# Kernel optimization log

Hardware: AMD Instinct MI355X
Metric: run time of the kernel (lower is better)

## Reference

```python
import jax, jax.numpy as jnp
import numpy as np

KERNEL_SIZE = 5
SIGMA_SPACE = 1.0
SIGMA_COLOR = 0.1
PAD = KERNEL_SIZE // 2


def make_spatial_kernel(kernel_size, sigma_space):
    r = kernel_size // 2
    coords = jnp.arange(-r, r + 1, dtype=jnp.float32)
    xx, yy = jnp.meshgrid(coords, coords, indexing='ij')
    return jnp.exp(-(xx ** 2 + yy ** 2) / (2.0 * sigma_space ** 2))  # [K, K]


def setup_inputs() -> dict:
    key = jax.random.key(0)
    x = jax.random.uniform(key, (4, 3, 512, 512), dtype=jnp.float32)
    spatial_kernel = make_spatial_kernel(KERNEL_SIZE, SIGMA_SPACE)
    sigma_color = jnp.float32(SIGMA_COLOR)
    return {"x": x, "spatial_kernel": spatial_kernel, "sigma_color": sigma_color}


def reference(x, spatial_kernel, sigma_color):
    # x: [B, C, H, W]; spatial_kernel: [K, K] (fixed buffer, computed at init)
    B, C, H, W = x.shape
    K = KERNEL_SIZE
    padded = jnp.pad(x, ((0, 0), (0, 0), (PAD, PAD), (PAD, PAD)), mode='reflect')
    # Gather KxK windows as a trailing tap axis: [B, C, H, W, K*K]
    patches = jnp.stack(
        [padded[:, :, i:i + H, j:j + W] for i in range(K) for j in range(K)],
        axis=-1,
    )
    sk = spatial_kernel.reshape(-1)  # [K*K]
    color_diff = patches - x[..., None]
    color_weight = jnp.exp(-(color_diff ** 2) / (2.0 * sigma_color ** 2))
    weight = sk * color_weight  # [B, C, H, W, K*K]
    weight = weight / (jnp.sum(weight, axis=-1, keepdims=True) + 1e-8)
    return jnp.sum(weight * patches, axis=-1)  # [B, C, H, W]
```

## Files before the change

kernel.cpp:

```cpp
#include <hip/hip_runtime.h>

typedef float v2f __attribute__((ext_vector_type(2)));

constexpr int H = 512, W = 512;
constexpr int K = 5, PADR = 2;

__global__ void prep_kernel(const float* __restrict__ sk,
                            const float* __restrict__ sigma_color,
                            float* __restrict__ lw) {
    int t = threadIdx.x;
    if (t < K * K) lw[t] = __builtin_amdgcn_logf(sk[t]);
    if (t == K * K) {
        float s = sigma_color[0];
        lw[K * K] = -1.4426950408889634f / (2.0f * s * s);
    }
}

__global__ __launch_bounds__(256) void bilateral_kernel(
    const float* __restrict__ x,
    const float* __restrict__ lw,
    float* __restrict__ out)
{
    float c2 = lw[K * K];

    int t = threadIdx.x;
    int gid = blockIdx.x * 256 + t;
    int p0 = gid << 2;
    int w0 = p0 & (W - 1);
    int row = p0 >> 9;
    int h = row & (H - 1);
    int plane = row >> 9;
    const float* xp = x + (size_t)plane * (H * W);

    int hoff[K];
#pragma unroll
    for (int i = 0; i < K; ++i) {
        int hv = h + i - PADR;
        hv = (hv < 0) ? -hv : hv;
        hv = (hv >= H) ? (2 * H - 2 - hv) : hv;
        hoff[i] = hv << 9;
    }
    int wl0 = w0 - 2; wl0 = (wl0 < 0) ? -wl0 : wl0;
    int wl1 = w0 - 1; wl1 = (wl1 < 0) ? -wl1 : wl1;
    int wr0 = w0 + 4; wr0 = (wr0 >= W) ? (2 * W - 2 - wr0) : wr0;
    int wr1 = w0 + 5; wr1 = (wr1 >= W) ? (2 * W - 2 - wr1) : wr1;

    float win[K][8];
#pragma unroll
    for (int i = 0; i < K; ++i) {
        const float* rp = xp + hoff[i];
        float4 m = *(const float4*)(rp + w0);
        win[i][2] = m.x; win[i][3] = m.y; win[i][4] = m.z; win[i][5] = m.w;
        win[i][0] = rp[wl0];
        win[i][1] = rp[wl1];
        win[i][6] = rp[wr0];
        win[i][7] = rp[wr1];
    }

    v2f cA = { win[2][2], win[2][3] };
    v2f cB = { win[2][4], win[2][5] };
    v2f wsA = {0.f, 0.f}, wsB = {0.f, 0.f};
    v2f accA = {0.f, 0.f}, accB = {0.f, 0.f};

#pragma unroll
    for (int i = 0; i < K; ++i) {
#pragma unroll
        for (int j = 0; j < K; ++j) {
            float lwv = lw[i * K + j];
            v2f lsp = { lwv, lwv };
            v2f vA = { win[i][j],     win[i][j + 1] };
            v2f vB = { win[i][j + 2], win[i][j + 3] };
            v2f dA = vA - cA;
            v2f dB = vB - cB;
            v2f aA = dA * c2;
            v2f aB = dB * c2;
            v2f argA = __builtin_elementwise_fma(aA, dA, lsp);
            v2f argB = __builtin_elementwise_fma(aB, dB, lsp);
            v2f wA, wB;
            wA[0] = __builtin_amdgcn_exp2f(argA[0]);
            wA[1] = __builtin_amdgcn_exp2f(argA[1]);
            wB[0] = __builtin_amdgcn_exp2f(argB[0]);
            wB[1] = __builtin_amdgcn_exp2f(argB[1]);
            wsA += wA;
            wsB += wB;
            accA = __builtin_elementwise_fma(wA, vA, accA);
            accB = __builtin_elementwise_fma(wB, vB, accB);
        }
    }

    float4 o;
    o.x = accA[0] * __builtin_amdgcn_rcpf(wsA[0] + 1e-8f);
    o.y = accA[1] * __builtin_amdgcn_rcpf(wsA[1] + 1e-8f);
    o.z = accB[0] * __builtin_amdgcn_rcpf(wsB[0] + 1e-8f);
    o.w = accB[1] * __builtin_amdgcn_rcpf(wsB[1] + 1e-8f);
    *(float4*)(out + p0) = o;
}

extern "C" void kernel_launch(void* const* d_in, const int* in_sizes, int n_in,
                              void* d_out, int out_size, void* d_ws, size_t ws_size,
                              hipStream_t stream) {
    const float* x  = (const float*)d_in[0];
    const float* sk = (const float*)d_in[1];
    const float* sc = (const float*)d_in[2];
    float* out = (float*)d_out;
    float* lw  = (float*)d_ws;

    prep_kernel<<<1, 64, 0, stream>>>(sk, sc, lw);

    const int total = in_sizes[0];
    const int blocks = total / (256 * 4);
    bilateral_kernel<<<blocks, 256, 0, stream>>>(x, lw, out);
}
```

Before: 83.64 us.

## Fold prep kernel into main kernel using per-lane log and readlane broadcast

Removes the separate prep kernel launch. Each wavefront lane computes the log of one spatial weight and broadcasts it with readlane. It also switches the row loop to unroll 1, loading each row inside the loop instead of keeping the full 5x8 window in registers, which lowers register pressure. The costs are a serialized load-then-compute per row, which reduces memory-level parallelism, and a log plus a sigma read done redundantly in every thread.

```diff
diff --git a/kernel.cpp b/kernel.cpp
--- a/kernel.cpp
+++ b/kernel.cpp
@@ -5,25 +5,28 @@
 constexpr int H = 512, W = 512;
 constexpr int K = 5, PADR = 2;
 
-__global__ void prep_kernel(const float* __restrict__ sk,
-                            const float* __restrict__ sigma_color,
-                            float* __restrict__ lw) {
-    int t = threadIdx.x;
-    if (t < K * K) lw[t] = __builtin_amdgcn_logf(sk[t]);
-    if (t == K * K) {
-        float s = sigma_color[0];
-        lw[K * K] = -1.4426950408889634f / (2.0f * s * s);
-    }
+__device__ inline float readlane_f(float v, int l) {
+    union { float f; int i; } u; u.f = v;
+    u.i = __builtin_amdgcn_readlane(u.i, l);
+    return u.f;
 }
 
 __global__ __launch_bounds__(256) void bilateral_kernel(
     const float* __restrict__ x,
-    const float* __restrict__ lw,
+    const float* __restrict__ sk,
+    const float* __restrict__ sigma_color,
     float* __restrict__ out)
 {
-    float c2 = lw[K * K];
+    int t = threadIdx.x;
+    int lane = t & 63;
 
-    int t = threadIdx.x;
+    float skl = sk[lane < K * K ? lane : 0];
+    float vlog = __builtin_amdgcn_logf(skl);
+
+    float s = sigma_color[0];
+    float c2 = -1.4426950408889634f / (2.0f * s * s);
+    v2f c2v = { c2, c2 };
+
     int gid = blockIdx.x * 256 + t;
     int p0 = gid << 2;
     int w0 = p0 & (W - 1);
@@ -32,50 +35,42 @@
     int plane = row >> 9;
     const float* xp = x + (size_t)plane * (H * W);
 
-    int hoff[K];
-#pragma unroll
-    for (int i = 0; i < K; ++i) {
-        int hv = h + i - PADR;
-        hv = (hv < 0) ? -hv : hv;
-        hv = (hv >= H) ? (2 * H - 2 - hv) : hv;
-        hoff[i] = hv << 9;
-    }
     int wl0 = w0 - 2; wl0 = (wl0 < 0) ? -wl0 : wl0;
     int wl1 = w0 - 1; wl1 = (wl1 < 0) ? -wl1 : wl1;
     int wr0 = w0 + 4; wr0 = (wr0 >= W) ? (2 * W - 2 - wr0) : wr0;
     int wr1 = w0 + 5; wr1 = (wr1 >= W) ? (2 * W - 2 - wr1) : wr1;
 
-    float win[K][8];
-#pragma unroll
-    for (int i = 0; i < K; ++i) {
-        const float* rp = xp + hoff[i];
-        float4 m = *(const float4*)(rp + w0);
-        win[i][2] = m.x; win[i][3] = m.y; win[i][4] = m.z; win[i][5] = m.w;
-        win[i][0] = rp[wl0];
-        win[i][1] = rp[wl1];
-        win[i][6] = rp[wr0];
-        win[i][7] = rp[wr1];
-    }
-
-    v2f cA = { win[2][2], win[2][3] };
-    v2f cB = { win[2][4], win[2][5] };
+    float4 c = *(const float4*)(xp + (h << 9) + w0);
+    v2f cA = { c.x, c.y }, cB = { c.z, c.w };
     v2f wsA = {0.f, 0.f}, wsB = {0.f, 0.f};
     v2f accA = {0.f, 0.f}, accB = {0.f, 0.f};
 
-#pragma unroll
+#pragma unroll 1
     for (int i = 0; i < K; ++i) {
+        int hv = h + i - PADR;
+        hv = (hv < 0) ? -hv : hv;
+        hv = (hv >= H) ? (2 * H - 2 - hv) : hv;
+        const float* rp = xp + (hv << 9);
+
+        float rowv[8];
+        float4 m = *(const float4*)(rp + w0);
+        rowv[0] = rp[wl0];
+        rowv[1] = rp[wl1];
+        rowv[2] = m.x; rowv[3] = m.y; rowv[4] = m.z; rowv[5] = m.w;
+        rowv[6] = rp[wr0];
+        rowv[7] = rp[wr1];
+
+        int lbase = i * K;
 #pragma unroll
         for (int j = 0; j < K; ++j) {
-            float lwv = lw[i * K + j];
+            float lwv = readlane_f(vlog, lbase + j);
             v2f lsp = { lwv, lwv };
-            v2f vA = { win[i][j],     win[i][j + 1] };
-            v2f vB = { win[i][j + 2], win[i][j + 3] };
+            v2f vA = { rowv[j],     rowv[j + 1] };
+            v2f vB = { rowv[j + 2], rowv[j + 3] };
             v2f dA = vA - cA;
             v2f dB = vB - cB;
-            v2f aA = dA * c2;
-            v2f aB = dB * c2;
-            v2f argA = __builtin_elementwise_fma(aA, dA, lsp);
-            v2f argB = __builtin_elementwise_fma(aB, dB, lsp);
+            v2f argA = __builtin_elementwise_fma(dA * c2v, dA, lsp);
+            v2f argB = __builtin_elementwise_fma(dB * c2v, dB, lsp);
             v2f wA, wB;
             wA[0] = __builtin_amdgcn_exp2f(argA[0]);
             wA[1] = __builtin_amdgcn_exp2f(argA[1]);
@@ -103,11 +98,8 @@
     const float* sk = (const float*)d_in[1];
     const float* sc = (const float*)d_in[2];
     float* out = (float*)d_out;
-    float* lw  = (float*)d_ws;
-
-    prep_kernel<<<1, 64, 0, stream>>>(sk, sc, lw);
 
     const int total = in_sizes[0];
     const int blocks = total / (256 * 4);
-    bilateral_kernel<<<blocks, 256, 0, stream>>>(x, lw, out);
+    bilateral_kernel<<<blocks, 256, 0, stream>>>(x, sk, sc, out);
 }
```

Result: no change. 84.47 us (+1.0%).
